# Kernel optimization log

Hardware: AMD Instinct MI355X
Metric: run time of the kernel (lower is better)

Reference implementation:

```python
import jax, jax.numpy as jnp
import numpy as np

B, T, D_IN, H, D_OUT = 32, 2048, 128, 256, 256


def setup_inputs() -> dict:
    key = jax.random.key(0)
    ks = jax.random.split(key, 12)
    sx = 1.0 / np.sqrt(D_IN)
    sh = 1.0 / np.sqrt(H)
    return {
        "x": jax.random.normal(ks[0], (B, T, D_IN), dtype=jnp.float32),
        "h0": jnp.zeros((B, H), dtype=jnp.float32),
        "Wz": jax.random.normal(ks[1], (D_IN, H), dtype=jnp.float32) * sx,
        "Uz": jax.random.normal(ks[2], (H, H), dtype=jnp.float32) * sh,
        "bz": jnp.zeros((H,), dtype=jnp.float32),
        "Wr": jax.random.normal(ks[3], (D_IN, H), dtype=jnp.float32) * sx,
        "Ur": jax.random.normal(ks[4], (H, H), dtype=jnp.float32) * sh,
        "br": jnp.zeros((H,), dtype=jnp.float32),
        "Wh": jax.random.normal(ks[5], (D_IN, H), dtype=jnp.float32) * sx,
        "Uh": jax.random.normal(ks[6], (H, H), dtype=jnp.float32) * sh,
        "bh": jnp.zeros((H,), dtype=jnp.float32),
        "Wo": jax.random.normal(ks[7], (H, D_OUT), dtype=jnp.float32) * sh,
        "bo": jnp.zeros((D_OUT,), dtype=jnp.float32),
    }


def reference(x, h0, Wz, Uz, bz, Wr, Ur, br, Wh, Uh, bh, Wo, bo):
    # TimeDistributed: swap [B,T,*] -> [T,B,*], loop cell over time collecting
    # every cell output per step, swap back. Here the cell is a GRU emitting
    # (y_t, h_t) with h_t also carried as the recurrent state.
    def step(h, xt):  # xt: [B, D_IN], h: [B, H]
        z = jax.nn.sigmoid(xt @ Wz + h @ Uz + bz)
        r = jax.nn.sigmoid(xt @ Wr + h @ Ur + br)
        hh = jnp.tanh(xt @ Wh + (r * h) @ Uh + bh)
        hn = (1.0 - z) * h + z * hh
        y = hn @ Wo + bo
        return hn, (y, hn)

    xT = jnp.swapaxes(x, 0, 1)  # [T, B, D_IN]
    _, (ys, hs) = jax.lax.scan(step, h0, xT)
    # stack back to batch-major: [B, T, D_OUT], [B, T, H]
    return jnp.swapaxes(ys, 0, 1), jnp.swapaxes(hs, 0, 1)
```

## Files before the change

kernel.cpp:

```cpp
#include <hip/hip_runtime.h>

#define B_   32
#define T_   2048
#define DIN  128
#define H_   256
#define DOUT 256

typedef _Float16 h2_t __attribute__((ext_vector_type(2)));

__device__ __forceinline__ float fdot2a(unsigned int a, unsigned int b, float c) {
#if defined(__has_builtin) && __has_builtin(__builtin_amdgcn_fdot2)
  return __builtin_amdgcn_fdot2(__builtin_bit_cast(h2_t, a),
                                __builtin_bit_cast(h2_t, b), c, false);
#else
  h2_t x = __builtin_bit_cast(h2_t, a), y = __builtin_bit_cast(h2_t, b);
  return c + (float)x[0] * (float)y[0] + (float)x[1] * (float)y[1];
#endif
}

__device__ __forceinline__ float dot256(const unsigned int* uc, const uint4* hp) {
  float a0 = 0.f, a1 = 0.f, a2 = 0.f, a3 = 0.f;
#pragma unroll
  for (int k8 = 0; k8 < 32; ++k8) {
    uint4 hq = hp[k8];
    a0 = fdot2a(uc[4 * k8 + 0], hq.x, a0);
    a1 = fdot2a(uc[4 * k8 + 1], hq.y, a1);
    a2 = fdot2a(uc[4 * k8 + 2], hq.z, a2);
    a3 = fdot2a(uc[4 * k8 + 3], hq.w, a3);
  }
  return (a0 + a1) + (a2 + a3);
}

__device__ __forceinline__ float dot128(const unsigned int* uc, const uint4* hp) {
  float a0 = 0.f, a1 = 0.f, a2 = 0.f, a3 = 0.f;
#pragma unroll
  for (int k8 = 0; k8 < 16; ++k8) {
    uint4 hq = hp[k8];
    a0 = fdot2a(uc[4 * k8 + 0], hq.x, a0);
    a1 = fdot2a(uc[4 * k8 + 1], hq.y, a1);
    a2 = fdot2a(uc[4 * k8 + 2], hq.z, a2);
    a3 = fdot2a(uc[4 * k8 + 3], hq.w, a3);
  }
  return (a0 + a1) + (a2 + a3);
}

__global__ __launch_bounds__(256) void k_gates(
    const float* __restrict__ x,
    const float* __restrict__ Wz, const float* __restrict__ Wr,
    const float* __restrict__ Wh,
    const float* __restrict__ bz, const float* __restrict__ br,
    const float* __restrict__ bh,
    _Float16* __restrict__ Gzr,
    _Float16* __restrict__ Gh)
{
  __shared__ __align__(16) float sx[32][DIN];
  const int gate = blockIdx.y;
  const float* W = (gate == 0) ? Wz : (gate == 1) ? Wr : Wh;
  const float* bias = (gate == 0) ? bz : (gate == 1) ? br : bh;
  const int row0 = blockIdx.x * 32;
  const int tid = threadIdx.x;

  const float4* xg = (const float4*)(x + (size_t)row0 * DIN);
  float4* sx4 = (float4*)&sx[0][0];
#pragma unroll
  for (int m = 0; m < 4; ++m) sx4[tid + 256 * m] = xg[tid + 256 * m];
  __syncthreads();

  const int j = tid;
  const float bj = bias[j];
  float acc[32];
#pragma unroll
  for (int i = 0; i < 32; ++i) acc[i] = 0.f;

#pragma unroll 2
  for (int k4 = 0; k4 < DIN / 4; ++k4) {
    float w0 = W[(size_t)(4 * k4 + 0) * H_ + j];
    float w1 = W[(size_t)(4 * k4 + 1) * H_ + j];
    float w2 = W[(size_t)(4 * k4 + 2) * H_ + j];
    float w3 = W[(size_t)(4 * k4 + 3) * H_ + j];
#pragma unroll
    for (int i = 0; i < 32; ++i) {
      float4 xv = *(const float4*)&sx[i][4 * k4];
      acc[i] = fmaf(xv.x, w0, acc[i]);
      acc[i] = fmaf(xv.y, w1, acc[i]);
      acc[i] = fmaf(xv.z, w2, acc[i]);
      acc[i] = fmaf(xv.w, w3, acc[i]);
    }
  }

  if (gate < 2) {
    _Float16* Gp = Gzr + (size_t)row0 * 512 + gate * H_ + j;
#pragma unroll
    for (int i = 0; i < 32; ++i) Gp[(size_t)i * 512] = (_Float16)(acc[i] + bj);
  } else {
    _Float16* Gp = Gh + (size_t)row0 * H_ + j;
#pragma unroll
    for (int i = 0; i < 32; ++i) Gp[(size_t)i * H_] = (_Float16)(acc[i] + bj);
  }
}

__global__ __launch_bounds__(512, 2) void k_scan(
    const float* __restrict__ h0,
    const float* __restrict__ Uz, const float* __restrict__ Ur,
    const float* __restrict__ Uh,
    const _Float16* __restrict__ Gzr, const _Float16* __restrict__ Gh,
    float* __restrict__ hs)
{
  __shared__ __align__(16) _Float16 h_h[H_];
  __shared__ __align__(16) _Float16 rh_h[H_];
  __shared__ float h_f[H_];
  __shared__ float z_s[H_];
  __shared__ float ph_s[H_];

  const int b = blockIdx.x;
  const int tid = threadIdx.x;
  const int half = tid >> 8;
  const int j = tid & 255;

  const float* Uzr = half ? Ur : Uz;
  unsigned int uzr[128];
#pragma unroll
  for (int k2 = 0; k2 < 128; ++k2) {
    float a = Uzr[(size_t)(2 * k2) * H_ + j];
    float c = Uzr[(size_t)(2 * k2 + 1) * H_ + j];
    h2_t p; p[0] = (_Float16)a; p[1] = (_Float16)c;
    uzr[k2] = __builtin_bit_cast(unsigned int, p);
  }
  unsigned int uh[64];
#pragma unroll
  for (int k2 = 0; k2 < 64; ++k2) {
    int k = half * 128 + 2 * k2;
    float a = Uh[(size_t)k * H_ + j];
    float c = Uh[(size_t)(k + 1) * H_ + j];
    h2_t p; p[0] = (_Float16)a; p[1] = (_Float16)c;
    uh[k2] = __builtin_bit_cast(unsigned int, p);
  }

  if (tid < H_) {
    float h = h0[(size_t)b * H_ + tid];
    h_f[tid] = h;
    h_h[tid] = (_Float16)h;
  }
  __syncthreads();

  const _Float16* Gzr_p = Gzr + (size_t)b * T_ * 512 + half * H_ + j;
  const _Float16* Gh_p  = Gh  + (size_t)b * T_ * H_ + j;
  _Float16 g_zr = Gzr_p[0];
  _Float16 g_h  = (half == 0) ? Gh_p[0] : (_Float16)0.f;

  float* hsb = hs + (size_t)b * T_ * H_;

#pragma unroll 1
  for (int t = 0; t < T_; ++t) {
    const float gv_zr = (float)g_zr;
    const float gv_h  = (float)g_h;
    const int tn = (t + 1 < T_) ? (t + 1) : t;
    g_zr = Gzr_p[(size_t)tn * 512];
    if (half == 0) g_h = Gh_p[(size_t)tn * H_];

    {
      float acc = dot256(uzr, (const uint4*)h_h);
      float s = 1.f / (1.f + __expf(-(gv_zr + acc)));
      if (half == 0) z_s[j] = s;
      else           rh_h[j] = (_Float16)(s * h_f[j]);
    }
    __syncthreads();

    {
      float p = dot128(uh, (const uint4*)rh_h + half * 16);
      if (half == 1) ph_s[j] = p;
      __syncthreads();
      if (half == 0) {
        float xh = gv_h + p + ph_s[j];
        float e = __expf(-2.f * xh);
        float hh = 2.f / (1.f + e) - 1.f;
        float z = z_s[j];
        float h = h_f[j];
        float hn = (1.f - z) * h + z * hh;
        h_f[j] = hn;
        h_h[j] = (_Float16)hn;
        hsb[(size_t)t * H_ + j] = hn;
      }
    }
    __syncthreads();
  }
}

__global__ __launch_bounds__(256) void k_out(
    const float* __restrict__ hs, const float* __restrict__ Wo,
    const float* __restrict__ bo, float* __restrict__ ys)
{
  __shared__ __align__(16) float sh[32][H_];
  const int row0 = blockIdx.x * 32;
  const int tid = threadIdx.x;

  const float4* hg = (const float4*)(hs + (size_t)row0 * H_);
  float4* sh4 = (float4*)&sh[0][0];
#pragma unroll
  for (int m = 0; m < 8; ++m) sh4[tid + 256 * m] = hg[tid + 256 * m];
  __syncthreads();

  const int j = tid;
  float acc[32];
#pragma unroll
  for (int i = 0; i < 32; ++i) acc[i] = 0.f;

#pragma unroll 2
  for (int k4 = 0; k4 < H_ / 4; ++k4) {
    float w0 = Wo[(size_t)(4 * k4 + 0) * DOUT + j];
    float w1 = Wo[(size_t)(4 * k4 + 1) * DOUT + j];
    float w2 = Wo[(size_t)(4 * k4 + 2) * DOUT + j];
    float w3 = Wo[(size_t)(4 * k4 + 3) * DOUT + j];
#pragma unroll
    for (int i = 0; i < 32; ++i) {
      float4 hv = *(const float4*)&sh[i][4 * k4];
      acc[i] = fmaf(hv.x, w0, acc[i]);
      acc[i] = fmaf(hv.y, w1, acc[i]);
      acc[i] = fmaf(hv.z, w2, acc[i]);
      acc[i] = fmaf(hv.w, w3, acc[i]);
    }
  }

  const float bj = bo[j];
  float* yp = ys + (size_t)row0 * DOUT + j;
#pragma unroll
  for (int i = 0; i < 32; ++i) yp[(size_t)i * DOUT] = acc[i] + bj;
}

extern "C" void kernel_launch(void* const* d_in, const int* in_sizes, int n_in,
                              void* d_out, int out_size, void* d_ws, size_t ws_size,
                              hipStream_t stream) {
  const float* x  = (const float*)d_in[0];
  const float* h0 = (const float*)d_in[1];
  const float* Wz = (const float*)d_in[2];
  const float* Uz = (const float*)d_in[3];
  const float* bz = (const float*)d_in[4];
  const float* Wr = (const float*)d_in[5];
  const float* Ur = (const float*)d_in[6];
  const float* br = (const float*)d_in[7];
  const float* Wh = (const float*)d_in[8];
  const float* Uh = (const float*)d_in[9];
  const float* bh = (const float*)d_in[10];
  const float* Wo = (const float*)d_in[11];
  const float* bo = (const float*)d_in[12];

  float* ys = (float*)d_out;
  float* hsO = ys + (size_t)B_ * T_ * DOUT;

  _Float16* Gzr = (_Float16*)d_out;
  _Float16* Gh  = (_Float16*)d_ws;

  dim3 g1((B_ * T_) / 32, 3);
  k_gates<<<g1, 256, 0, stream>>>(x, Wz, Wr, Wh, bz, br, bh, Gzr, Gh);
  k_scan<<<B_, 512, 0, stream>>>(h0, Uz, Ur, Uh, Gzr, Gh, hsO);
  k_out<<<(B_ * T_) / 32, 256, 0, stream>>>(hsO, Wo, bo, ys);
}
```

Measured before the change: 3.515 ms.

## Split GRU scan recurrent matvecs across 1024 threads with K-quarter partial sums

```diff
diff --git a/kernel.cpp b/kernel.cpp
--- a/kernel.cpp
+++ b/kernel.cpp
@@ -16,32 +16,6 @@
   h2_t x = __builtin_bit_cast(h2_t, a), y = __builtin_bit_cast(h2_t, b);
   return c + (float)x[0] * (float)y[0] + (float)x[1] * (float)y[1];
 #endif
-}
-
-__device__ __forceinline__ float dot256(const unsigned int* uc, const uint4* hp) {
-  float a0 = 0.f, a1 = 0.f, a2 = 0.f, a3 = 0.f;
-#pragma unroll
-  for (int k8 = 0; k8 < 32; ++k8) {
-    uint4 hq = hp[k8];
-    a0 = fdot2a(uc[4 * k8 + 0], hq.x, a0);
-    a1 = fdot2a(uc[4 * k8 + 1], hq.y, a1);
-    a2 = fdot2a(uc[4 * k8 + 2], hq.z, a2);
-    a3 = fdot2a(uc[4 * k8 + 3], hq.w, a3);
-  }
-  return (a0 + a1) + (a2 + a3);
-}
-
-__device__ __forceinline__ float dot128(const unsigned int* uc, const uint4* hp) {
-  float a0 = 0.f, a1 = 0.f, a2 = 0.f, a3 = 0.f;
-#pragma unroll
-  for (int k8 = 0; k8 < 16; ++k8) {
-    uint4 hq = hp[k8];
-    a0 = fdot2a(uc[4 * k8 + 0], hq.x, a0);
-    a1 = fdot2a(uc[4 * k8 + 1], hq.y, a1);
-    a2 = fdot2a(uc[4 * k8 + 2], hq.z, a2);
-    a3 = fdot2a(uc[4 * k8 + 3], hq.w, a3);
-  }
-  return (a0 + a1) + (a2 + a3);
 }
 
 __global__ __launch_bounds__(256) void k_gates(
@@ -99,7 +73,9 @@
   }
 }
 
-__global__ __launch_bounds__(512, 2) void k_scan(
+__global__
+__attribute__((amdgpu_flat_work_group_size(1024, 1024), amdgpu_waves_per_eu(4, 4)))
+void k_scan(
     const float* __restrict__ h0,
     const float* __restrict__ Uz, const float* __restrict__ Ur,
     const float* __restrict__ Uh,
@@ -109,78 +85,128 @@
   __shared__ __align__(16) _Float16 h_h[H_];
   __shared__ __align__(16) _Float16 rh_h[H_];
   __shared__ float h_f[H_];
-  __shared__ float z_s[H_];
-  __shared__ float ph_s[H_];
+  __shared__ float zp[4][H_];
+  __shared__ float rp[4][H_];
 
   const int b = blockIdx.x;
   const int tid = threadIdx.x;
-  const int half = tid >> 8;
   const int j = tid & 255;
-
-  const float* Uzr = half ? Ur : Uz;
-  unsigned int uzr[128];
-#pragma unroll
-  for (int k2 = 0; k2 < 128; ++k2) {
-    float a = Uzr[(size_t)(2 * k2) * H_ + j];
-    float c = Uzr[(size_t)(2 * k2 + 1) * H_ + j];
-    h2_t p; p[0] = (_Float16)a; p[1] = (_Float16)c;
-    uzr[k2] = __builtin_bit_cast(unsigned int, p);
-  }
-  unsigned int uh[64];
-#pragma unroll
-  for (int k2 = 0; k2 < 64; ++k2) {
-    int k = half * 128 + 2 * k2;
-    float a = Uh[(size_t)k * H_ + j];
-    float c = Uh[(size_t)(k + 1) * H_ + j];
-    h2_t p; p[0] = (_Float16)a; p[1] = (_Float16)c;
-    uh[k2] = __builtin_bit_cast(unsigned int, p);
-  }
-
+  const int kq = tid >> 8;
+  const int k0 = kq * 64;
+
+  unsigned int uz[32], ur[32], uh[32];
+#pragma unroll
+  for (int m = 0; m < 32; ++m) {
+    int k = k0 + 2 * m;
+    {
+      float a = Uz[(size_t)k * H_ + j], c = Uz[(size_t)(k + 1) * H_ + j];
+      h2_t p; p[0] = (_Float16)a; p[1] = (_Float16)c;
+      uz[m] = __builtin_bit_cast(unsigned int, p);
+    }
+    {
+      float a = Ur[(size_t)k * H_ + j], c = Ur[(size_t)(k + 1) * H_ + j];
+      h2_t p; p[0] = (_Float16)a; p[1] = (_Float16)c;
+      ur[m] = __builtin_bit_cast(unsigned int, p);
+    }
+    {
+      float a = Uh[(size_t)k * H_ + j], c = Uh[(size_t)(k + 1) * H_ + j];
+      h2_t p; p[0] = (_Float16)a; p[1] = (_Float16)c;
+      uh[m] = __builtin_bit_cast(unsigned int, p);
+    }
+  }
+#pragma unroll
+  for (int m = 0; m < 32; ++m) {
+    asm volatile("" : "+v"(uz[m]));
+    asm volatile("" : "+v"(ur[m]));
+    asm volatile("" : "+v"(uh[m]));
+  }
+
+  float hreg = 0.f;
   if (tid < H_) {
-    float h = h0[(size_t)b * H_ + tid];
-    h_f[tid] = h;
-    h_h[tid] = (_Float16)h;
+    hreg = h0[(size_t)b * H_ + tid];
+    h_f[tid] = hreg;
+    h_h[tid] = (_Float16)hreg;
   }
   __syncthreads();
 
-  const _Float16* Gzr_p = Gzr + (size_t)b * T_ * 512 + half * H_ + j;
+  const _Float16* Gzr_p = Gzr + (size_t)b * T_ * 512 + tid;
   const _Float16* Gh_p  = Gh  + (size_t)b * T_ * H_ + j;
-  _Float16 g_zr = Gzr_p[0];
-  _Float16 g_h  = (half == 0) ? Gh_p[0] : (_Float16)0.f;
+  float g_zr = 0.f, g_h = 0.f;
+  if (tid < 512) g_zr = (float)Gzr_p[0];
+  if (tid < 256) g_h  = (float)Gh_p[0];
 
   float* hsb = hs + (size_t)b * T_ * H_;
+  float zreg = 0.f;
+
+  const uint4* hq4  = (const uint4*)h_h  + kq * 8;
+  const uint4* rhq4 = (const uint4*)rh_h + kq * 8;
 
 #pragma unroll 1
   for (int t = 0; t < T_; ++t) {
-    const float gv_zr = (float)g_zr;
-    const float gv_h  = (float)g_h;
+    const float gv_zr = g_zr;
+    const float gv_h  = g_h;
     const int tn = (t + 1 < T_) ? (t + 1) : t;
-    g_zr = Gzr_p[(size_t)tn * 512];
-    if (half == 0) g_h = Gh_p[(size_t)tn * H_];
-
-    {
-      float acc = dot256(uzr, (const uint4*)h_h);
-      float s = 1.f / (1.f + __expf(-(gv_zr + acc)));
-      if (half == 0) z_s[j] = s;
-      else           rh_h[j] = (_Float16)(s * h_f[j]);
-    }
-    __syncthreads();
-
-    {
-      float p = dot128(uh, (const uint4*)rh_h + half * 16);
-      if (half == 1) ph_s[j] = p;
-      __syncthreads();
-      if (half == 0) {
-        float xh = gv_h + p + ph_s[j];
-        float e = __expf(-2.f * xh);
-        float hh = 2.f / (1.f + e) - 1.f;
-        float z = z_s[j];
-        float h = h_f[j];
-        float hn = (1.f - z) * h + z * hh;
-        h_f[j] = hn;
-        h_h[j] = (_Float16)hn;
-        hsb[(size_t)t * H_ + j] = hn;
+    if (tid < 512) g_zr = (float)Gzr_p[tn * 512];
+    if (tid < 256) g_h  = (float)Gh_p[tn * H_];
+
+    {
+      float za0 = 0.f, za1 = 0.f, za2 = 0.f, za3 = 0.f;
+      float ra0 = 0.f, ra1 = 0.f, ra2 = 0.f, ra3 = 0.f;
+#pragma unroll
+      for (int m = 0; m < 8; ++m) {
+        uint4 hq = hq4[m];
+        za0 = fdot2a(uz[4 * m + 0], hq.x, za0);
+        za1 = fdot2a(uz[4 * m + 1], hq.y, za1);
+        za2 = fdot2a(uz[4 * m + 2], hq.z, za2);
+        za3 = fdot2a(uz[4 * m + 3], hq.w, za3);
+        ra0 = fdot2a(ur[4 * m + 0], hq.x, ra0);
+        ra1 = fdot2a(ur[4 * m + 1], hq.y, ra1);
+        ra2 = fdot2a(ur[4 * m + 2], hq.z, ra2);
+        ra3 = fdot2a(ur[4 * m + 3], hq.w, ra3);
       }
+      zp[kq][j] = (za0 + za1) + (za2 + za3);
+      rp[kq][j] = (ra0 + ra1) + (ra2 + ra3);
+    }
+    __syncthreads();
+
+    if (tid < 512) {
+      const float* P = (tid < 256) ? &zp[0][0] : &rp[0][0];
+      float s4 = (P[j] + P[H_ + j]) + (P[2 * H_ + j] + P[3 * H_ + j]);
+      float e = __expf(-(gv_zr + s4));
+      float s = __builtin_amdgcn_rcpf(1.f + e);
+      if (tid < 256) {
+        zreg = s;
+      } else {
+        rh_h[j] = (_Float16)(s * h_f[j]);
+      }
+    }
+    __syncthreads();
+
+    {
+      float ha0 = 0.f, ha1 = 0.f, ha2 = 0.f, ha3 = 0.f;
+#pragma unroll
+      for (int m = 0; m < 8; ++m) {
+        uint4 hq = rhq4[m];
+        ha0 = fdot2a(uh[4 * m + 0], hq.x, ha0);
+        ha1 = fdot2a(uh[4 * m + 1], hq.y, ha1);
+        ha2 = fdot2a(uh[4 * m + 2], hq.z, ha2);
+        ha3 = fdot2a(uh[4 * m + 3], hq.w, ha3);
+      }
+      zp[kq][j] = (ha0 + ha1) + (ha2 + ha3);
+    }
+    __syncthreads();
+
+    if (tid < 256) {
+      const float* P = &zp[0][0];
+      float s4 = (P[j] + P[H_ + j]) + (P[2 * H_ + j] + P[3 * H_ + j]);
+      float xh = gv_h + s4;
+      float e = __expf(-2.f * xh);
+      float hh = 2.f * __builtin_amdgcn_rcpf(1.f + e) - 1.f;
+      float hn = (1.f - zreg) * hreg + zreg * hh;
+      hreg = hn;
+      h_f[j] = hn;
+      h_h[j] = (_Float16)hn;
+      hsb[t * H_ + j] = hn;
     }
     __syncthreads();
   }
@@ -252,6 +278,6 @@
 
   dim3 g1((B_ * T_) / 32, 3);
   k_gates<<<g1, 256, 0, stream>>>(x, Wz, Wr, Wh, bz, br, bh, Gzr, Gh);
-  k_scan<<<B_, 512, 0, stream>>>(h0, Uz, Ur, Uh, Gzr, Gh, hsO);
+  k_scan<<<B_, 1024, 0, stream>>>(h0, Uz, Ur, Uh, Gzr, Gh, hsO);
   k_out<<<(B_ * T_) / 32, 256, 0, stream>>>(hsO, Wo, bo, ys);
 }
```

Measured after the change: 5.300 ms. 50.8% more time.
